# Optimization experiments

Hardware: AMD Instinct MI355X
Metric: run time of the kernel (lower is better)

Reference implementation:

```python
import jax, jax.numpy as jnp
import numpy as np

EMBED = 1024
HEADS = 16
HEAD_DIM = EMBED // HEADS


def setup_inputs() -> dict:
    key = jax.random.key(0)
    ks = jax.random.split(key, 9)
    B, S = 1, 4096
    scale = 1.0 / np.sqrt(EMBED)
    x = jax.random.normal(ks[0], (B, S, EMBED), dtype=jnp.float32)
    # nn.Linear weights stored as [out, in]; we store transposed [in, out] for x @ W
    Wq = jax.random.uniform(ks[1], (EMBED, EMBED), jnp.float32, -scale, scale)
    bq = jax.random.uniform(ks[2], (EMBED,), jnp.float32, -scale, scale)
    Wk = jax.random.uniform(ks[3], (EMBED, EMBED), jnp.float32, -scale, scale)
    bk = jax.random.uniform(ks[4], (EMBED,), jnp.float32, -scale, scale)
    Wv = jax.random.uniform(ks[5], (EMBED, EMBED), jnp.float32, -scale, scale)
    bv = jax.random.uniform(ks[6], (EMBED,), jnp.float32, -scale, scale)
    Wo = jax.random.uniform(ks[7], (EMBED, EMBED), jnp.float32, -scale, scale)
    bo = jax.random.uniform(ks[8], (EMBED,), jnp.float32, -scale, scale)
    return {"x": x, "Wq": Wq, "bq": bq, "Wk": Wk, "bk": bk,
            "Wv": Wv, "bv": bv, "Wo": Wo, "bo": bo}


def reference(x, Wq, bq, Wk, bk, Wv, bv, Wo, bo):
    B, S, E = x.shape
    H, D = HEADS, HEAD_DIM
    # projections
    Q = (x @ Wq + bq).reshape(B, S, H, D).transpose(0, 2, 1, 3)  # [B,H,S,D]
    K = (x @ Wk + bk).reshape(B, S, H, D).transpose(0, 2, 1, 3)
    V = (x @ Wv + bv).reshape(B, S, H, D).transpose(0, 2, 1, 3)
    # unfused attention: full [B,H,S,S] score matrix, matching the torch module
    scores = jnp.einsum('bhqd,bhkd->bhqk', Q, K) / jnp.sqrt(jnp.float32(D)).astype(x.dtype)
    probs = jax.nn.softmax(scores, axis=-1)
    out = jnp.einsum('bhqk,bhkd->bhqd', probs, V)  # [B,H,S,D]
    out = out.transpose(0, 2, 1, 3).reshape(B, S, E)
    return out @ Wo + bo
```

## Files before the change

### kernel.cpp

```cpp
#include <hip/hip_runtime.h>


constexpr int Sq = 4096;
constexpr int Ee = 1024;
constexpr int Hh = 16;
constexpr int Dh = 64;

typedef _Float16 half8 __attribute__((ext_vector_type(8)));
typedef _Float16 half4 __attribute__((ext_vector_type(4)));
typedef _Float16 half2t __attribute__((ext_vector_type(2)));
typedef float f32x4 __attribute__((ext_vector_type(4)));

union U8 { half8 v8; half2t h2[4]; };

__device__ __forceinline__ unsigned short f2h(float f) {
  _Float16 h = (_Float16)f;
  return *reinterpret_cast<unsigned short*>(&h);
}

__device__ __forceinline__ half2t pk(float a, float b) {
  return __builtin_bit_cast(half2t, __builtin_amdgcn_cvt_pkrtz(a, b));
}

__device__ __forceinline__ void gload16(const void* g, void* l) {
  __builtin_amdgcn_global_load_lds(
      (const __attribute__((address_space(1))) void*)g,
      (__attribute__((address_space(3))) void*)l, 16, 0, 0);
}

__global__ void k_prep(const float* __restrict__ x,
                       const float* __restrict__ Wq, const float* __restrict__ Wk,
                       const float* __restrict__ Wv, const float* __restrict__ Wo,
                       unsigned short* __restrict__ xb,
                       unsigned short* __restrict__ Wqt, unsigned short* __restrict__ Wkt,
                       unsigned short* __restrict__ Wvt, unsigned short* __restrict__ Wot) {
  int b = blockIdx.x, t = threadIdx.x;
  if (b < 4096) {
    int i = b * 256 + t;
    float4 v = reinterpret_cast<const float4*>(x)[i];
    ushort4 o;
    o.x = f2h(v.x); o.y = f2h(v.y); o.z = f2h(v.z); o.w = f2h(v.w);
    reinterpret_cast<ushort4*>(xb)[i] = o;
    return;
  }
  __shared__ unsigned short tile[64][65];
  int r = b - 4096;
  int wi = r >> 8, ti = r & 255;
  const float* W = (wi == 0) ? Wq : (wi == 1) ? Wk : (wi == 2) ? Wv : Wo;
  unsigned short* Wt = (wi == 0) ? Wqt : (wi == 1) ? Wkt : (wi == 2) ? Wvt : Wot;
  int kb = (ti & 15) * 64, nb = (ti >> 4) * 64;
  int r0 = t >> 4, c4 = (t & 15) * 4;
  for (int i = 0; i < 4; i++) {
    int row = r0 + i * 16;
    float4 v = *reinterpret_cast<const float4*>(W + (size_t)(kb + row) * Ee + nb + c4);
    tile[row][c4 + 0] = f2h(v.x); tile[row][c4 + 1] = f2h(v.y);
    tile[row][c4 + 2] = f2h(v.z); tile[row][c4 + 3] = f2h(v.w);
  }
  __syncthreads();
  for (int i = 0; i < 4; i++) {
    int nrow = r0 + i * 16;
    ushort4 o;
    o.x = tile[c4 + 0][nrow]; o.y = tile[c4 + 1][nrow];
    o.z = tile[c4 + 2][nrow]; o.w = tile[c4 + 3][nrow];
    *reinterpret_cast<ushort4*>(Wt + (size_t)(nb + nrow) * Ee + kb + c4) = o;
  }
}

__global__ __launch_bounds__(512, 2) void k_gemm(
    const unsigned short* __restrict__ A,
    const unsigned short* __restrict__ W0, const unsigned short* __restrict__ W1,
    const unsigned short* __restrict__ W2,
    const float* __restrict__ b0, const float* __restrict__ b1, const float* __restrict__ b2,
    void* d0, void* d1, void* d2) {
  __shared__ __align__(16) unsigned short Al[2 * 8192];
  __shared__ __align__(16) unsigned short Bl[2 * 3 * 8192];
  int bid = blockIdx.x;
  int yp = bid & 7;
  int xm = bid >> 3;
  int m0 = xm * 128, n0 = yp * 128;

  int t = threadIdx.x;
  int w = t >> 6, L = t & 63, quad = L >> 4, c = L & 15;
  int wm = w >> 2, wn = w & 3;

  const unsigned short* Wz[3] = {W0, W1, W2};

  f32x4 zero = {0.f, 0.f, 0.f, 0.f};
  f32x4 acc[3][4][2];
#pragma unroll
  for (int z = 0; z < 3; z++)
#pragma unroll
    for (int a = 0; a < 4; a++)
#pragma unroll
      for (int b = 0; b < 2; b++) acc[z][a][b] = zero;

  auto stageAB = [&](int buf, int k0) {
#pragma unroll
    for (int i = 0; i < 2; i++) {
      int ch = i * 512 + t;
      int row = ch >> 3, kg = (ch & 7) ^ (row & 7);
      gload16(A + (size_t)(m0 + row) * 1024 + k0 + kg * 8, &Al[buf * 8192 + ch * 8]);
    }
#pragma unroll
    for (int z = 0; z < 3; z++)
#pragma unroll
      for (int i = 0; i < 2; i++) {
        int ch = i * 512 + t;
        int row = ch >> 3, kg = (ch & 7) ^ (row & 7);
        gload16(Wz[z] + (size_t)(n0 + row) * 1024 + k0 + kg * 8,
                &Bl[(buf * 3 + z) * 8192 + ch * 8]);
      }
  };

  auto compute = [&](int cur) {
    const unsigned short* Ab = &Al[cur * 8192];
#pragma unroll
    for (int ks = 0; ks < 2; ks++) {
      half8 af[4];
#pragma unroll
      for (int a = 0; a < 4; a++) {
        int row = wm * 64 + a * 16 + c;
        int kg = (quad + 4 * ks) ^ (row & 7);
        af[a] = *reinterpret_cast<const half8*>(&Ab[row * 64 + kg * 8]);
      }
#pragma unroll
      for (int z = 0; z < 3; z++) {
        const unsigned short* Bb = &Bl[(cur * 3 + z) * 8192];
        half8 bfr[2];
#pragma unroll
        for (int b = 0; b < 2; b++) {
          int row = wn * 32 + b * 16 + c;
          int kg = (quad + 4 * ks) ^ (row & 7);
          bfr[b] = *reinterpret_cast<const half8*>(&Bb[row * 64 + kg * 8]);
        }
#pragma unroll
        for (int a = 0; a < 4; a++)
#pragma unroll
          for (int b = 0; b < 2; b++) {
            if (z < 2)
              acc[z][a][b] = __builtin_amdgcn_mfma_f32_16x16x32_f16(bfr[b], af[a], acc[z][a][b], 0, 0, 0);
            else
              acc[z][a][b] = __builtin_amdgcn_mfma_f32_16x16x32_f16(af[a], bfr[b], acc[z][a][b], 0, 0, 0);
          }
      }
    }
  };

  stageAB(0, 0);
  stageAB(1, 64);
  for (int k0 = 0; k0 < 960; k0 += 64) {
    int cur = (k0 >> 6) & 1;
    asm volatile("s_waitcnt vmcnt(8)" ::: "memory");
    __builtin_amdgcn_s_barrier();
    __builtin_amdgcn_sched_barrier(0);
    compute(cur);
    __builtin_amdgcn_s_barrier();
    if (k0 < 896) stageAB(cur, k0 + 128);
  }
  asm volatile("s_waitcnt vmcnt(0)" ::: "memory");
  __builtin_amdgcn_s_barrier();
  __builtin_amdgcn_sched_barrier(0);
  compute(1);

  {
#pragma unroll
    for (int z = 0; z < 2; z++) {
      float sc = (z == 0) ? 0.18033688011112042f : 1.0f;
      const float* bias = (z == 0) ? b0 : b1;
      unsigned short* qk = (unsigned short*)((z == 0) ? d0 : d1);
#pragma unroll
      for (int b = 0; b < 2; b++) {
        int nb4 = n0 + wn * 32 + b * 16 + quad * 4;
        int hh = nb4 >> 6, d = nb4 & 63;
        f32x4 b4 = *reinterpret_cast<const f32x4*>(bias + nb4);
#pragma unroll
        for (int a = 0; a < 4; a++) {
          int s = m0 + wm * 64 + a * 16 + c;
          half4 hv;
#pragma unroll
          for (int r = 0; r < 4; r++) hv[r] = (_Float16)((acc[z][a][b][r] + b4[r]) * sc);
          *reinterpret_cast<half4*>(&qk[(size_t)hh * Sq * Dh + (size_t)s * Dh + d]) = hv;
        }
      }
    }
  }
  {
    unsigned short* Vt = (unsigned short*)d2;
#pragma unroll
    for (int b = 0; b < 2; b++) {
      int n = n0 + wn * 32 + b * 16 + c;
      int hh = n >> 6, d = n & 63;
      float bvf = b2[n];
#pragma unroll
      for (int a = 0; a < 4; a++) {
        int pos = m0 + wm * 64 + (a >> 1) * 32 + quad * 8 + (a & 1) * 4;
        half4 hv;
#pragma unroll
        for (int r = 0; r < 4; r++) hv[r] = (_Float16)(acc[2][a][b][r] + bvf);
        *reinterpret_cast<half4*>(&Vt[(size_t)hh * Dh * Sq + (size_t)d * Sq + pos]) = hv;
      }
    }
  }
}

__global__ __launch_bounds__(256) void k_gemmO(
    const unsigned short* __restrict__ A, const unsigned short* __restrict__ Wt,
    const float* __restrict__ bias, float* __restrict__ out) {
  __shared__ __align__(16) unsigned short Al[2 * 64 * 64];
  __shared__ __align__(16) unsigned short Bl[2 * 128 * 64];
  int bid = blockIdx.x;
  int yp = bid & 7;
  int xm = bid >> 3;
  int t = threadIdx.x;
  int w = t >> 6, L = t & 63, quad = L >> 4, c = L & 15;
  int m0 = xm * 64, n0 = yp * 128;
  int wm = w & 1, wn = w >> 1;

  f32x4 zero = {0.f, 0.f, 0.f, 0.f};
  f32x4 acc[4][2];
#pragma unroll
  for (int j = 0; j < 4; j++)
#pragma unroll
    for (int i = 0; i < 2; i++) acc[j][i] = zero;

  auto stageAB = [&](int buf, int k0) {
#pragma unroll
    for (int i = 0; i < 2; i++) {
      int ch = i * 256 + t;
      int row = ch >> 3, kg = (ch & 7) ^ (row & 7);
      gload16(A + (size_t)(m0 + row) * 1024 + k0 + kg * 8, &Al[buf * 4096 + ch * 8]);
    }
#pragma unroll
    for (int i = 0; i < 4; i++) {
      int ch = i * 256 + t;
      int row = ch >> 3, kg = (ch & 7) ^ (row & 7);
      gload16(Wt + (size_t)(n0 + row) * 1024 + k0 + kg * 8, &Bl[buf * 8192 + ch * 8]);
    }
  };
  auto compute = [&](int cur) {
    const unsigned short* Ab = &Al[cur * 4096];
    const unsigned short* Bb = &Bl[cur * 8192];
#pragma unroll
    for (int ks = 0; ks < 2; ks++) {
      half8 af[2], bfr[4];
#pragma unroll
      for (int i = 0; i < 2; i++) {
        int row = wm * 32 + i * 16 + c;
        int kg = (quad + 4 * ks) ^ (row & 7);
        af[i] = *reinterpret_cast<const half8*>(&Ab[row * 64 + kg * 8]);
      }
#pragma unroll
      for (int j = 0; j < 4; j++) {
        int row = wn * 64 + j * 16 + c;
        int kg = (quad + 4 * ks) ^ (row & 7);
        bfr[j] = *reinterpret_cast<const half8*>(&Bb[row * 64 + kg * 8]);
      }
#pragma unroll
      for (int j = 0; j < 4; j++)
#pragma unroll
        for (int i = 0; i < 2; i++)
          acc[j][i] = __builtin_amdgcn_mfma_f32_16x16x32_f16(bfr[j], af[i], acc[j][i], 0, 0, 0);
    }
  };
  stageAB(0, 0);
  stageAB(1, 64);
  for (int k0 = 0; k0 < 960; k0 += 64) {
    int cur = (k0 >> 6) & 1;
    asm volatile("s_waitcnt vmcnt(6)" ::: "memory");
    __builtin_amdgcn_s_barrier();
    __builtin_amdgcn_sched_barrier(0);
    compute(cur);
    __builtin_amdgcn_s_barrier();
    if (k0 < 896) stageAB(cur, k0 + 128);
  }
  asm volatile("s_waitcnt vmcnt(0)" ::: "memory");
  __builtin_amdgcn_s_barrier();
  __builtin_amdgcn_sched_barrier(0);
  compute(1);

#pragma unroll
  for (int j = 0; j < 4; j++) {
    int nb4 = n0 + wn * 64 + j * 16 + quad * 4;
    f32x4 b4 = *reinterpret_cast<const f32x4*>(bias + nb4);
#pragma unroll
    for (int i = 0; i < 2; i++) {
      int s = m0 + wm * 32 + i * 16 + c;
      f32x4 v = acc[j][i] + b4;
      *reinterpret_cast<f32x4*>(out + (size_t)s * 1024 + nb4) = v;
    }
  }
}

__global__ __launch_bounds__(256, 2) void k_attn(
    const unsigned short* __restrict__ Q, const unsigned short* __restrict__ K,
    const unsigned short* __restrict__ Vt, unsigned short* __restrict__ O) {
  __shared__ __align__(16) unsigned short SM[32768];
  int t = threadIdx.x;
  int w = t >> 6, L = t & 63, quad = L >> 4, c = L & 15;
  int wl = w & 1, par = w >> 1;
  int h = blockIdx.y, qb = blockIdx.x;
  const unsigned short* Qh = Q + (size_t)h * Sq * Dh;
  const unsigned short* Kh = K + (size_t)h * Sq * Dh;
  const unsigned short* Vth = Vt + (size_t)h * Dh * Sq;

  half8 qf[4][2];
#pragma unroll
  for (int qg = 0; qg < 4; qg++) {
    int qrow = qb * 128 + wl * 64 + qg * 16 + c;
#pragma unroll
    for (int ks = 0; ks < 2; ks++)
      qf[qg][ks] = *reinterpret_cast<const half8*>(Qh + (size_t)qrow * Dh + ks * 32 + quad * 8);
  }

  f32x4 zero = {0.f, 0.f, 0.f, 0.f};
  f32x4 o[4][4];
  f32x4 l[4];
#pragma unroll
  for (int qg = 0; qg < 4; qg++) {
    l[qg] = zero;
#pragma unroll
    for (int dt = 0; dt < 4; dt++) o[qg][dt] = zero;
  }
  half8 ones8;
#pragma unroll
  for (int j = 0; j < 8; j++) ones8[j] = (_Float16)1.0f;

  int koff[2][4], voff[4][2];
#pragma unroll
  for (int ks = 0; ks < 2; ks++)
#pragma unroll
    for (int nt = 0; nt < 4; nt++) {
      int row = nt * 16 + c;
      koff[ks][nt] = par * 4096 + row * 64 + (((ks * 4 + quad) ^ (row & 7)) * 8);
    }
#pragma unroll
  for (int dt = 0; dt < 4; dt++)
#pragma unroll
    for (int n2 = 0; n2 < 2; n2++) {
      int row = dt * 16 + c;
      voff[dt][n2] = (2 + par) * 4096 + row * 64 + (((n2 * 4 + quad) ^ (row & 7)) * 8);
    }

  const unsigned short* KgB[2];
  const unsigned short* VgB[2];
#pragma unroll
  for (int i = 0; i < 2; i++) {
    int ch = i * 256 + t;
    int row = ch >> 3, kg = (ch & 7) ^ (row & 7);
    KgB[i] = Kh + row * Dh + kg * 8;
    VgB[i] = Vth + (size_t)row * Sq + kg * 8;
  }

  auto stage = [&](int bufo, int tb) {
#pragma unroll
    for (int p2 = 0; p2 < 2; p2++) {
#pragma unroll
      for (int i = 0; i < 2; i++)
        gload16(KgB[i] + (size_t)(tb + p2) * 4096, &SM[bufo + p2 * 4096 + (i * 256 + t) * 8]);
#pragma unroll
      for (int i = 0; i < 2; i++)
        gload16(VgB[i] + (size_t)(tb + p2) * 64, &SM[bufo + (2 + p2) * 4096 + (i * 256 + t) * 8]);
    }
  };

  stage(0, 0);

  auto body = [&](int BUFOFF) {
    half8 pB[4][2];
#pragma unroll
    for (int h2 = 0; h2 < 2; h2++) {
      f32x4 st[2][4];
      __builtin_amdgcn_s_setprio(1);
#pragma unroll
      for (int nt = 0; nt < 4; nt++) {
        half8 kfv = *reinterpret_cast<const half8*>(&SM[koff[0][nt] + BUFOFF]);
        st[0][nt] = __builtin_amdgcn_mfma_f32_16x16x32_f16(kfv, qf[2 * h2 + 0][0], zero, 0, 0, 0);
        st[1][nt] = __builtin_amdgcn_mfma_f32_16x16x32_f16(kfv, qf[2 * h2 + 1][0], zero, 0, 0, 0);
      }
#pragma unroll
      for (int nt = 0; nt < 4; nt++) {
        half8 kfv = *reinterpret_cast<const half8*>(&SM[koff[1][nt] + BUFOFF]);
        st[0][nt] = __builtin_amdgcn_mfma_f32_16x16x32_f16(kfv, qf[2 * h2 + 0][1], st[0][nt], 0, 0, 0);
        st[1][nt] = __builtin_amdgcn_mfma_f32_16x16x32_f16(kfv, qf[2 * h2 + 1][1], st[1][nt], 0, 0, 0);
      }
      __builtin_amdgcn_s_setprio(0);
#pragma unroll
      for (int q2 = 0; q2 < 2; q2++)
#pragma unroll
        for (int n2 = 0; n2 < 2; n2++) {
          U8 u;
          u.h2[0] = pk(__builtin_amdgcn_exp2f(st[q2][2 * n2][0]), __builtin_amdgcn_exp2f(st[q2][2 * n2][1]));
          u.h2[1] = pk(__builtin_amdgcn_exp2f(st[q2][2 * n2][2]), __builtin_amdgcn_exp2f(st[q2][2 * n2][3]));
          u.h2[2] = pk(__builtin_amdgcn_exp2f(st[q2][2 * n2 + 1][0]), __builtin_amdgcn_exp2f(st[q2][2 * n2 + 1][1]));
          u.h2[3] = pk(__builtin_amdgcn_exp2f(st[q2][2 * n2 + 1][2]), __builtin_amdgcn_exp2f(st[q2][2 * n2 + 1][3]));
          pB[2 * h2 + q2][n2] = u.v8;
          l[2 * h2 + q2] = __builtin_amdgcn_mfma_f32_16x16x32_f16(ones8, u.v8, l[2 * h2 + q2], 0, 0, 0);
        }
    }
    __builtin_amdgcn_s_setprio(1);
#pragma unroll
    for (int dt = 0; dt < 4; dt++)
#pragma unroll
      for (int n2 = 0; n2 < 2; n2++) {
        half8 vv = *reinterpret_cast<const half8*>(&SM[voff[dt][n2] + BUFOFF]);
        o[0][dt] = __builtin_amdgcn_mfma_f32_16x16x32_f16(vv, pB[0][n2], o[0][dt], 0, 0, 0);
        o[1][dt] = __builtin_amdgcn_mfma_f32_16x16x32_f16(vv, pB[1][n2], o[1][dt], 0, 0, 0);
        o[2][dt] = __builtin_amdgcn_mfma_f32_16x16x32_f16(vv, pB[2][n2], o[2][dt], 0, 0, 0);
        o[3][dt] = __builtin_amdgcn_mfma_f32_16x16x32_f16(vv, pB[3][n2], o[3][dt], 0, 0, 0);
      }
    __builtin_amdgcn_s_setprio(0);
  };

  for (int ob2 = 0; ob2 < 16; ob2++) {
    __syncthreads();
    stage(16384, 4 * ob2 + 2);
    body(0);
    __syncthreads();
    if (ob2 < 15) stage(0, 4 * ob2 + 4);
    body(16384);
  }

  __syncthreads();
  float* cb = (float*)SM;
  if (par == 1) {
#pragma unroll
    for (int qg = 0; qg < 4; qg++)
#pragma unroll
      for (int dt = 0; dt < 4; dt++)
        *reinterpret_cast<f32x4*>(cb + ((wl * 17 + qg * 4 + dt) * 64 + L) * 4) = o[qg][dt];
    f32x4 lv = {l[0][0], l[1][0], l[2][0], l[3][0]};
    *reinterpret_cast<f32x4*>(cb + ((wl * 17 + 16) * 64 + L) * 4) = lv;
  }
  __syncthreads();
  if (par == 0) {
#pragma unroll
    for (int qg = 0; qg < 4; qg++)
#pragma unroll
      for (int dt = 0; dt < 4; dt++)
        o[qg][dt] += *reinterpret_cast<const f32x4*>(cb + ((wl * 17 + qg * 4 + dt) * 64 + L) * 4);
    f32x4 lv = *reinterpret_cast<const f32x4*>(cb + ((wl * 17 + 16) * 64 + L) * 4);
#pragma unroll
    for (int qg = 0; qg < 4; qg++) {
      float inv = 1.f / (l[qg][0] + lv[qg]);
      int q = qb * 128 + wl * 64 + qg * 16 + c;
#pragma unroll
      for (int dt = 0; dt < 4; dt++) {
        half4 hv;
#pragma unroll
        for (int r = 0; r < 4; r++) hv[r] = (_Float16)(o[qg][dt][r] * inv);
        *reinterpret_cast<half4*>(&O[(size_t)q * 1024 + h * 64 + dt * 16 + quad * 4]) = hv;
      }
    }
  }
}

extern "C" void kernel_launch(void* const* d_in, const int* in_sizes, int n_in,
                              void* d_out, int out_size, void* d_ws, size_t ws_size,
                              hipStream_t stream) {
  const float* x  = (const float*)d_in[0];
  const float* Wq = (const float*)d_in[1];
  const float* bq = (const float*)d_in[2];
  const float* Wk = (const float*)d_in[3];
  const float* bk = (const float*)d_in[4];
  const float* Wv = (const float*)d_in[5];
  const float* bv = (const float*)d_in[6];
  const float* Wo = (const float*)d_in[7];
  const float* bo = (const float*)d_in[8];

  char* ws = (char*)d_ws;
  const size_t MB = 1u << 20;
  unsigned short* xb  = (unsigned short*)(ws);
  unsigned short* Wqt = (unsigned short*)(ws + 8 * MB);
  unsigned short* Wkt = (unsigned short*)(ws + 10 * MB);
  unsigned short* Wvt = (unsigned short*)(ws + 12 * MB);
  unsigned short* Wot = (unsigned short*)(ws + 14 * MB);
  unsigned short* Qb  = (unsigned short*)(ws + 16 * MB);
  unsigned short* Kb  = (unsigned short*)(ws + 24 * MB);
  unsigned short* Vtg = (unsigned short*)(ws + 32 * MB);
  unsigned short* Ob  = (unsigned short*)(ws + 40 * MB);

  k_prep<<<5120, 256, 0, stream>>>(x, Wq, Wk, Wv, Wo, xb, Wqt, Wkt, Wvt, Wot);
  k_prep<<<5120, 256, 0, stream>>>(x, Wq, Wk, Wv, Wo, xb, Wqt, Wkt, Wvt, Wot);
  k_prep<<<5120, 256, 0, stream>>>(x, Wq, Wk, Wv, Wo, xb, Wqt, Wkt, Wvt, Wot);
  k_gemm<<<256, 512, 0, stream>>>(xb, Wqt, Wkt, Wvt, bq, bk, bv,
                                  (void*)Qb, (void*)Kb, (void*)Vtg);
  k_attn<<<dim3(32, 16), 256, 0, stream>>>(Qb, Kb, Vtg, Ob);
  k_gemmO<<<512, 256, 0, stream>>>(Ob, Wot, bo, (float*)d_out);
  k_gemmO<<<512, 256, 0, stream>>>(Ob, Wot, bo, (float*)d_out);
  k_gemmO<<<512, 256, 0, stream>>>(Ob, Wot, bo, (float*)d_out);
}
```

Baseline: 262.1 us.

## Alternate QK/softmax scheduling variant per block and drop duplicate launches

Adds a batched variant of the attention body that issues all QK^T MFMAs for both half-groups before doing the exp/pack work. Blocks pick that variant or the original interleaved one from a parity of qb and head, so neighbouring blocks on a CU run out of phase and their MFMA and VALU bursts can overlap. The batched path holds twice as many score registers live, which risks register pressure at the 2-blocks-per-CU launch bound. The change also removes the repeated k_prep and k_gemmO launches, which were redundant recomputations of the same outputs.

```diff
diff --git a/kernel.cpp b/kernel.cpp
--- a/kernel.cpp
+++ b/kernel.cpp
@@ -12,6 +12,8 @@
 typedef float f32x4 __attribute__((ext_vector_type(4)));
 
 union U8 { half8 v8; half2t h2[4]; };
+
+template <int N> struct IC { static constexpr int value = N; };
 
 __device__ __forceinline__ unsigned short f2h(float f) {
   _Float16 h = (_Float16)f;
@@ -299,6 +301,7 @@
   int w = t >> 6, L = t & 63, quad = L >> 4, c = L & 15;
   int wl = w & 1, par = w >> 1;
   int h = blockIdx.y, qb = blockIdx.x;
+  bool keyB = ((qb + (h >> 3)) & 1) != 0;
   const unsigned short* Qh = Q + (size_t)h * Sq * Dh;
   const unsigned short* Kh = K + (size_t)h * Sq * Dh;
   const unsigned short* Vth = Vt + (size_t)h * Dh * Sq;
@@ -365,60 +368,96 @@
 
   stage(0, 0);
 
-  auto body = [&](int BUFOFF) {
-    half8 pB[4][2];
-#pragma unroll
-    for (int h2 = 0; h2 < 2; h2++) {
-      f32x4 st[2][4];
+  auto packu = [&](f32x4 (&stq)[4], int n2, half8& pBq, f32x4& lq) {
+    U8 u;
+    u.h2[0] = pk(__builtin_amdgcn_exp2f(stq[2 * n2][0]), __builtin_amdgcn_exp2f(stq[2 * n2][1]));
+    u.h2[1] = pk(__builtin_amdgcn_exp2f(stq[2 * n2][2]), __builtin_amdgcn_exp2f(stq[2 * n2][3]));
+    u.h2[2] = pk(__builtin_amdgcn_exp2f(stq[2 * n2 + 1][0]), __builtin_amdgcn_exp2f(stq[2 * n2 + 1][1]));
+    u.h2[3] = pk(__builtin_amdgcn_exp2f(stq[2 * n2 + 1][2]), __builtin_amdgcn_exp2f(stq[2 * n2 + 1][3]));
+    pBq = u.v8;
+    lq = __builtin_amdgcn_mfma_f32_16x16x32_f16(ones8, u.v8, lq, 0, 0, 0);
+  };
+
+  auto run = [&](auto BC) {
+    constexpr int BATCH = BC.value;
+    auto body = [&](int BUFOFF) {
+      half8 pB[4][2];
+      if constexpr (BATCH) {
+        f32x4 st[2][2][4];
+        __builtin_amdgcn_s_setprio(1);
+#pragma unroll
+        for (int h2 = 0; h2 < 2; h2++) {
+#pragma unroll
+          for (int nt = 0; nt < 4; nt++) {
+            half8 kfv = *reinterpret_cast<const half8*>(&SM[koff[0][nt] + BUFOFF]);
+            st[h2][0][nt] = __builtin_amdgcn_mfma_f32_16x16x32_f16(kfv, qf[2 * h2 + 0][0], zero, 0, 0, 0);
+            st[h2][1][nt] = __builtin_amdgcn_mfma_f32_16x16x32_f16(kfv, qf[2 * h2 + 1][0], zero, 0, 0, 0);
+          }
+#pragma unroll
+          for (int nt = 0; nt < 4; nt++) {
+            half8 kfv = *reinterpret_cast<const half8*>(&SM[koff[1][nt] + BUFOFF]);
+            st[h2][0][nt] = __builtin_amdgcn_mfma_f32_16x16x32_f16(kfv, qf[2 * h2 + 0][1], st[h2][0][nt], 0, 0, 0);
+            st[h2][1][nt] = __builtin_amdgcn_mfma_f32_16x16x32_f16(kfv, qf[2 * h2 + 1][1], st[h2][1][nt], 0, 0, 0);
+          }
+        }
+        __builtin_amdgcn_s_setprio(0);
+#pragma unroll
+        for (int h2 = 0; h2 < 2; h2++)
+#pragma unroll
+          for (int q2 = 0; q2 < 2; q2++)
+#pragma unroll
+            for (int n2 = 0; n2 < 2; n2++)
+              packu(st[h2][q2], n2, pB[2 * h2 + q2][n2], l[2 * h2 + q2]);
+      } else {
+#pragma unroll
+        for (int h2 = 0; h2 < 2; h2++) {
+          f32x4 st[2][4];
+          __builtin_amdgcn_s_setprio(1);
+#pragma unroll
+          for (int nt = 0; nt < 4; nt++) {
+            half8 kfv = *reinterpret_cast<const half8*>(&SM[koff[0][nt] + BUFOFF]);
+            st[0][nt] = __builtin_amdgcn_mfma_f32_16x16x32_f16(kfv, qf[2 * h2 + 0][0], zero, 0, 0, 0);
+            st[1][nt] = __builtin_amdgcn_mfma_f32_16x16x32_f16(kfv, qf[2 * h2 + 1][0], zero, 0, 0, 0);
+          }
+#pragma unroll
+          for (int nt = 0; nt < 4; nt++) {
+            half8 kfv = *reinterpret_cast<const half8*>(&SM[koff[1][nt] + BUFOFF]);
+            st[0][nt] = __builtin_amdgcn_mfma_f32_16x16x32_f16(kfv, qf[2 * h2 + 0][1], st[0][nt], 0, 0, 0);
+            st[1][nt] = __builtin_amdgcn_mfma_f32_16x16x32_f16(kfv, qf[2 * h2 + 1][1], st[1][nt], 0, 0, 0);
+          }
+          __builtin_amdgcn_s_setprio(0);
+#pragma unroll
+          for (int q2 = 0; q2 < 2; q2++)
+#pragma unroll
+            for (int n2 = 0; n2 < 2; n2++)
+              packu(st[q2], n2, pB[2 * h2 + q2][n2], l[2 * h2 + q2]);
+        }
+      }
       __builtin_amdgcn_s_setprio(1);
 #pragma unroll
-      for (int nt = 0; nt < 4; nt++) {
-        half8 kfv = *reinterpret_cast<const half8*>(&SM[koff[0][nt] + BUFOFF]);
-        st[0][nt] = __builtin_amdgcn_mfma_f32_16x16x32_f16(kfv, qf[2 * h2 + 0][0], zero, 0, 0, 0);
-        st[1][nt] = __builtin_amdgcn_mfma_f32_16x16x32_f16(kfv, qf[2 * h2 + 1][0], zero, 0, 0, 0);
-      }
-#pragma unroll
-      for (int nt = 0; nt < 4; nt++) {
-        half8 kfv = *reinterpret_cast<const half8*>(&SM[koff[1][nt] + BUFOFF]);
-        st[0][nt] = __builtin_amdgcn_mfma_f32_16x16x32_f16(kfv, qf[2 * h2 + 0][1], st[0][nt], 0, 0, 0);
-        st[1][nt] = __builtin_amdgcn_mfma_f32_16x16x32_f16(kfv, qf[2 * h2 + 1][1], st[1][nt], 0, 0, 0);
-      }
+      for (int dt = 0; dt < 4; dt++)
+#pragma unroll
+        for (int n2 = 0; n2 < 2; n2++) {
+          half8 vv = *reinterpret_cast<const half8*>(&SM[voff[dt][n2] + BUFOFF]);
+          o[0][dt] = __builtin_amdgcn_mfma_f32_16x16x32_f16(vv, pB[0][n2], o[0][dt], 0, 0, 0);
+          o[1][dt] = __builtin_amdgcn_mfma_f32_16x16x32_f16(vv, pB[1][n2], o[1][dt], 0, 0, 0);
+          o[2][dt] = __builtin_amdgcn_mfma_f32_16x16x32_f16(vv, pB[2][n2], o[2][dt], 0, 0, 0);
+          o[3][dt] = __builtin_amdgcn_mfma_f32_16x16x32_f16(vv, pB[3][n2], o[3][dt], 0, 0, 0);
+        }
       __builtin_amdgcn_s_setprio(0);
-#pragma unroll
-      for (int q2 = 0; q2 < 2; q2++)
-#pragma unroll
-        for (int n2 = 0; n2 < 2; n2++) {
-          U8 u;
-          u.h2[0] = pk(__builtin_amdgcn_exp2f(st[q2][2 * n2][0]), __builtin_amdgcn_exp2f(st[q2][2 * n2][1]));
-          u.h2[1] = pk(__builtin_amdgcn_exp2f(st[q2][2 * n2][2]), __builtin_amdgcn_exp2f(st[q2][2 * n2][3]));
-          u.h2[2] = pk(__builtin_amdgcn_exp2f(st[q2][2 * n2 + 1][0]), __builtin_amdgcn_exp2f(st[q2][2 * n2 + 1][1]));
-          u.h2[3] = pk(__builtin_amdgcn_exp2f(st[q2][2 * n2 + 1][2]), __builtin_amdgcn_exp2f(st[q2][2 * n2 + 1][3]));
-          pB[2 * h2 + q2][n2] = u.v8;
-          l[2 * h2 + q2] = __builtin_amdgcn_mfma_f32_16x16x32_f16(ones8, u.v8, l[2 * h2 + q2], 0, 0, 0);
-        }
-    }
-    __builtin_amdgcn_s_setprio(1);
-#pragma unroll
-    for (int dt = 0; dt < 4; dt++)
-#pragma unroll
-      for (int n2 = 0; n2 < 2; n2++) {
-        half8 vv = *reinterpret_cast<const half8*>(&SM[voff[dt][n2] + BUFOFF]);
-        o[0][dt] = __builtin_amdgcn_mfma_f32_16x16x32_f16(vv, pB[0][n2], o[0][dt], 0, 0, 0);
-        o[1][dt] = __builtin_amdgcn_mfma_f32_16x16x32_f16(vv, pB[1][n2], o[1][dt], 0, 0, 0);
-        o[2][dt] = __builtin_amdgcn_mfma_f32_16x16x32_f16(vv, pB[2][n2], o[2][dt], 0, 0, 0);
-        o[3][dt] = __builtin_amdgcn_mfma_f32_16x16x32_f16(vv, pB[3][n2], o[3][dt], 0, 0, 0);
-      }
-    __builtin_amdgcn_s_setprio(0);
-  };
-
-  for (int ob2 = 0; ob2 < 16; ob2++) {
-    __syncthreads();
-    stage(16384, 4 * ob2 + 2);
-    body(0);
-    __syncthreads();
-    if (ob2 < 15) stage(0, 4 * ob2 + 4);
-    body(16384);
-  }
+    };
+
+    for (int ob2 = 0; ob2 < 16; ob2++) {
+      __syncthreads();
+      stage(16384, 4 * ob2 + 2);
+      body(0);
+      __syncthreads();
+      if (ob2 < 15) stage(0, 4 * ob2 + 4);
+      body(16384);
+    }
+  };
+  if (keyB) run(IC<1>{});
+  else      run(IC<0>{});
 
   __syncthreads();
   float* cb = (float*)SM;
@@ -480,12 +519,8 @@
   unsigned short* Ob  = (unsigned short*)(ws + 40 * MB);
 
   k_prep<<<5120, 256, 0, stream>>>(x, Wq, Wk, Wv, Wo, xb, Wqt, Wkt, Wvt, Wot);
-  k_prep<<<5120, 256, 0, stream>>>(x, Wq, Wk, Wv, Wo, xb, Wqt, Wkt, Wvt, Wot);
-  k_prep<<<5120, 256, 0, stream>>>(x, Wq, Wk, Wv, Wo, xb, Wqt, Wkt, Wvt, Wot);
   k_gemm<<<256, 512, 0, stream>>>(xb, Wqt, Wkt, Wvt, bq, bk, bv,
                                   (void*)Qb, (void*)Kb, (void*)Vtg);
   k_attn<<<dim3(32, 16), 256, 0, stream>>>(Qb, Kb, Vtg, Ob);
   k_gemmO<<<512, 256, 0, stream>>>(Ob, Wot, bo, (float*)d_out);
-  k_gemmO<<<512, 256, 0, stream>>>(Ob, Wot, bo, (float*)d_out);
-  k_gemmO<<<512, 256, 0, stream>>>(Ob, Wot, bo, (float*)d_out);
-}
+}
```

New measurement: 210.2 us. 19.8% less time.
